# Optimization experiments

Hardware: AMD Instinct MI355X
Metric: run time of the kernel (lower is better)

Reference implementation:

```python
import jax, jax.numpy as jnp
from jax import lax
import numpy as np

B, C, L = 32, 8, 512
C_IN = 512      # must equal L (tokenConv consumes permuted tensor)
D_MODEL = 512
SCALE_NUM = 64  # 63 actual scales


def build_wavelet_bank(scale_num, LB=-8.0, UB=8.0, N=1024, Fb=2.0, Fc=8.0):
    """Replicates cmor_torch; returns centered zero-padded kernel bank [S, K].
    Zero-centering is exact because every kernel length (16*s+1) is odd and K is odd,
    so the padded conv with pad=(K-1)//2 equals the original per-scale conv with
    pad=(k-1)//2."""
    x = np.linspace(LB, UB, N)
    wav = (np.pi * Fb) ** (-0.5) * np.exp(2j * np.pi * Fc * x) * np.exp(-x ** 2 / Fb)
    step = x[1] - x[0]
    kernels = []
    for scale in np.arange(1, scale_num):
        j = (np.arange(scale * (x[-1] - x[0]) + 1) / (scale * step)).astype(int)
        j = j[j < wav.size]
        kernels.append(np.real(wav[j]) * scale ** (-0.5))
    K = max(len(k) for k in kernels)
    if K % 2 == 0:
        K += 1
    bank = np.zeros((len(kernels), K), np.float32)
    for i, k in enumerate(kernels):
        assert (K - len(k)) % 2 == 0, "kernel parity mismatch"
        off = (K - len(k)) // 2
        bank[i, off:off + len(k)] = k
    return bank


def setup_inputs() -> dict:
    key = jax.random.key(0)
    k1, k2 = jax.random.split(key)
    x = jax.random.normal(k1, (B, C, L), dtype=jnp.float32)
    wavelet_bank = jnp.asarray(build_wavelet_bank(SCALE_NUM))  # [63, K]
    token_w = jax.random.normal(k2, (D_MODEL, C_IN, 3), dtype=jnp.float32) * 0.02
    return {"x": x, "wavelet_bank": wavelet_bank, "token_w": token_w}


def reference(x, wavelet_bank, token_w):
    Bb, Cc, Ll = x.shape
    S, K = wavelet_bank.shape
    pad = (K - 1) // 2
    # fused CWT over all (channel, scale) pairs: [B*C, 1, L] conv [S, 1, K] -> [B*C, S, L]
    xr = x.reshape(Bb * Cc, 1, Ll)
    conv = lax.conv_general_dilated(
        xr, wavelet_bank[:, None, :], window_strides=(1,),
        padding=[(pad, pad)], dimension_numbers=("NCH", "OIH", "NCH"))
    d = jnp.abs(jnp.diff(conv, axis=-1))                 # [B*C, S, L-1]
    d = jnp.concatenate([d, d[..., -1:]], axis=-1)       # replicate last sample -> L
    feats = d.reshape(Bb, Cc * S, Ll)
    out = jnp.concatenate([x, feats], axis=1)            # [B, C*(1+S), L]
    # tokenConv on permuted tensor: channels = L (= c_in), length = C*(1+S)
    h = out.transpose(0, 2, 1)                           # [B, L, C_total]
    hp = jnp.concatenate([h[..., -1:], h, h[..., :1]], axis=-1)  # circular pad=1
    y = lax.conv_general_dilated(
        hp, token_w, window_strides=(1,), padding="VALID",
        dimension_numbers=("NCH", "OIH", "NCH"))         # [B, d_model, C_total]
    return y.transpose(0, 2, 1)                          # [B, C_total, d_model]
```

## Files before the change

kernel.cpp:

```cpp
#include <hip/hip_runtime.h>
#include <hip/hip_bf16.h>

#define NB 32
#define NC 8
#define NL 512
#define NS 63
#define NK 1009
#define NPAD 504
#define ND 512
#define NCT 512
#define NROWS 514

typedef __attribute__((ext_vector_type(4))) float f32x4;
typedef __attribute__((ext_vector_type(8))) short short8;

#define APAD_BYTES (NB * NROWS * NL * 2)
#define WB_BYTES   (3 * ND * NL * 2)

typedef const __attribute__((address_space(1))) unsigned int* gp1_t;
typedef __attribute__((address_space(3))) unsigned int* lp3_t;
__device__ __forceinline__ void gload_lds16(const void* g, void* l) {
  __builtin_amdgcn_global_load_lds((gp1_t)g, (lp3_t)l, 16, 0, 0);
}

__device__ __forceinline__ unsigned short bf16_bits(float v) {
  return __builtin_bit_cast(unsigned short, __float2bfloat16(v));
}

#define WAITVM(N) asm volatile("s_waitcnt vmcnt(" #N ")" ::: "memory")
#define FENCE() asm volatile("" ::: "memory")
#define BAR() __builtin_amdgcn_s_barrier()

__global__ __launch_bounds__(256) void prep_kernel(
    const float* __restrict__ bank, const float* __restrict__ tw,
    __hip_bfloat16* __restrict__ Wb, __hip_bfloat16* __restrict__ bankB) {
  const int idx = blockIdx.x * 256 + threadIdx.x;

  {
    int i0 = idx * 4;
    const float4* t4 = (const float4*)(tw + (size_t)i0 * 3);
    float4 a = t4[0], bq = t4[1], c4 = t4[2];
    ushort4 w0 = make_ushort4(bf16_bits(a.x), bf16_bits(a.w), bf16_bits(bq.z), bf16_bits(c4.y));
    ushort4 w1 = make_ushort4(bf16_bits(a.y), bf16_bits(bq.x), bf16_bits(bq.w), bf16_bits(c4.z));
    ushort4 w2 = make_ushort4(bf16_bits(a.z), bf16_bits(bq.y), bf16_bits(c4.x), bf16_bits(c4.w));
    *(ushort4*)(Wb + 0 * ND * NL + i0) = w0;
    *(ushort4*)(Wb + 1 * ND * NL + i0) = w1;
    *(ushort4*)(Wb + 2 * ND * NL + i0) = w2;
  }
  {
    int s = idx >> 10, k = idx & 1023;
    float v = (s < NS && k < NK) ? bank[s * NK + k] : 0.f;
    bankB[idx] = __float2bfloat16(v);
  }
}

#define CPY8_STRIDE 3152

__global__ __launch_bounds__(512) void cwt_kernel(
    const float* __restrict__ x, const __hip_bfloat16* __restrict__ bankB,
    __hip_bfloat16* __restrict__ Apad) {
  __shared__ __align__(16) char smem[8 * 16384 + 8 * CPY8_STRIDE];
  char* bankS = smem;
  char* cpy = smem + 8 * 16384;

  const int tid = threadIdx.x;
  const int bc = blockIdx.x;
  const int b = bc >> 3, c = bc & 7;
  const int w = tid >> 6, l = tid & 63;
  const int hi = l >> 4, li = l & 15;
  const int r8 = l & 7;

  const float* xrow = x + bc * NL;

  if (tid < 512) {
    __hip_bfloat16 v = __float2bfloat16(xrow[tid]);
    Apad[((size_t)(b * NROWS) + 1 + c) * NL + tid] = v;
    if (c == 0) Apad[((size_t)(b * NROWS) + 513) * NL + tid] = v;
  }

  for (int i = 0; i < 13; ++i) {
    int p = tid + i * 512;
    if (p < 6176) {
      int r_ = p / 772;
      int pe = p - r_ * 772;
      int g0 = 2 * pe;
      int i0 = g0 - 8 + r_;
      float xa = (i0 >= NPAD && i0 < NPAD + NL) ? xrow[i0 - NPAD] : 0.f;
      float xb = (i0 + 1 >= NPAD && i0 + 1 < NPAD + NL) ? xrow[i0 + 1 - NPAD] : 0.f;
      float xc = (i0 + 2 >= NPAD && i0 + 2 < NPAD + NL) ? xrow[i0 + 2 - NPAD] : 0.f;
      unsigned u = (unsigned)bf16_bits(xb - xa) | ((unsigned)bf16_bits(xc - xb) << 16);
      *(unsigned*)(cpy + r_ * CPY8_STRIDE + g0 * 2) = u;
    }
  }

#define STAGE(kt)                                                             \
  {                                                                           \
    for (int i = 0; i < 2; ++i) {                                             \
      int ck = tid + i * 512;                                                 \
      int s_ = ck >> 4, rb = ck & 15;                                         \
      int srcc = rb ^ (s_ & 7);                                               \
      gload_lds16(bankB + s_ * 1024 + (kt) * 128 + srcc * 8,                  \
                  bankS + (kt) * 16384 + ck * 16);                            \
    }                                                                         \
  }

#define AVMM(kt, ksl, m)                                                       \
  {                                                                            \
    int srow = (m) * 16 + li;                                                  \
    int chunk = ((ksl) * 4 + hi) ^ (srow & 7);                                 \
    short8 av = *(const short8*)(bankS + (kt) * 16384 + srow * 256 + chunk * 16); \
    _Pragma("unroll") for (int n = 0; n < 4; ++n)                              \
      acc[m][n] = __builtin_amdgcn_mfma_f32_16x16x32_bf16(av, bv[n],           \
                                                          acc[m][n], 0, 0, 0); \
  }

#define CCOMP(kt, M0, M1, M2, M3)                                              \
  {                                                                            \
    _Pragma("unroll") for (int ksl = 0; ksl < 4; ++ksl) {                      \
      short8 bv[4];                                                            \
      _Pragma("unroll") for (int n = 0; n < 4; ++n) {                          \
        int ebyte = 16 + 2 * (tbase + n * 16 + 8 * (li >> 3) +                 \
                              (kt) * 128 + ksl * 32 + 8 * hi);                 \
        bv[n] = *(const short8*)(cpy + r8 * CPY8_STRIDE + ebyte);              \
      }                                                                        \
      if (M0) AVMM(kt, ksl, 0);                                                \
      if (M1) AVMM(kt, ksl, 1);                                                \
      if (M2) AVMM(kt, ksl, 2);                                                \
      if (M3) AVMM(kt, ksl, 3);                                                \
    }                                                                          \
  }

  STAGE(0); STAGE(1); STAGE(2); STAGE(3);
  STAGE(4); STAGE(5); STAGE(6); STAGE(7);

  f32x4 acc[4][4] = {};
  const int tbase = w * 64;

  asm volatile("s_waitcnt vmcnt(14) lgkmcnt(0)" ::: "memory");
  BAR(); FENCE(); CCOMP(0, 0, 0, 1, 1);
  WAITVM(12); BAR(); FENCE(); CCOMP(1, 0, 1, 1, 1);
  WAITVM(10); BAR(); FENCE(); CCOMP(2, 1, 1, 1, 1);
  WAITVM(8);  BAR(); FENCE(); CCOMP(3, 1, 1, 1, 1);
  WAITVM(6);  BAR(); FENCE(); CCOMP(4, 1, 1, 1, 1);
  WAITVM(4);  BAR(); FENCE(); CCOMP(5, 0, 1, 1, 1);
  WAITVM(2);  BAR(); FENCE(); CCOMP(6, 0, 0, 1, 1);
  WAITVM(0);  BAR(); FENCE(); CCOMP(7, 0, 0, 0, 1);

#pragma unroll
  for (int m = 0; m < 4; ++m) {
#pragma unroll
    for (int rg = 0; rg < 4; ++rg) {
      int s = m * 16 + hi * 4 + rg;
      if (s >= NS) continue;
      int ch = 8 + c * NS + s;
      size_t rowbase = ((size_t)(b * NROWS) + 1 + ch) * NL;
#pragma unroll
      for (int n = 0; n < 4; ++n) {
        int t = tbase + n * 16 + li;
        float d = fabsf(acc[m][n][rg]);
        __hip_bfloat16 hv = __float2bfloat16(d);
        bool lastgrp = (w == 7 && n == 3);
        bool skip = lastgrp && (li == 15);
        bool dup = lastgrp && (li == 14);
        if (!skip) Apad[rowbase + t] = hv;
        if (dup) Apad[rowbase + 511] = hv;
        if (ch == NCT - 1) {
          size_t wrapbase = (size_t)(b * NROWS) * NL;
          if (!skip) Apad[wrapbase + t] = hv;
          if (dup) Apad[wrapbase + 511] = hv;
        }
      }
    }
  }
#undef STAGE
#undef AVMM
#undef CCOMP
}

__global__ __launch_bounds__(256) void gemm_kernel(
    const __hip_bfloat16* __restrict__ Ap, const __hip_bfloat16* __restrict__ Wb,
    float* __restrict__ out) {
  __shared__ __hip_bfloat16 sA[4][128 * 32];
  __shared__ __hip_bfloat16 sB[4][128 * 32];

  const int tid = threadIdx.x;
  const int gid = blockIdx.x;
  const int q = gid >> 3;
  const int pid = (gid & 7) * 16 + (q >> 2);
  const int b = pid >> 2;
  const int p0 = (pid & 3) * 128;
  const int o0 = (q & 3) * 128;

  const int w = tid >> 6, lane = tid & 63;
  const int wm = w >> 1, wn = w & 1;
  const int row_in = lane & 15, hi = lane >> 4;

  const int r0 = tid >> 2, cg0 = (tid & 3) ^ ((r0 >> 1) & 3);
  const int ck1 = tid + 256;
  const int r1 = ck1 >> 2, cg1 = (ck1 & 3) ^ ((r1 >> 1) & 3);

#define GSTAGE(kk, bu)                                                         \
  {                                                                            \
    const int kap_ = (kk) >> 4;                                                \
    const int l0_ = ((kk) & 15) << 5;                                          \
    gload_lds16(Ap + ((b * NROWS + p0 + kap_ + r0) * NL + l0_ + cg0 * 8),      \
                &sA[bu][tid * 8]);                                             \
    gload_lds16(Ap + ((b * NROWS + p0 + kap_ + r1) * NL + l0_ + cg1 * 8),      \
                &sA[bu][ck1 * 8]);                                             \
    gload_lds16(Wb + ((kap_ * ND + o0 + r0) * NL + l0_ + cg0 * 8),             \
                &sB[bu][tid * 8]);                                             \
    gload_lds16(Wb + ((kap_ * ND + o0 + r1) * NL + l0_ + cg1 * 8),             \
                &sB[bu][ck1 * 8]);                                             \
  }

#define COMPUTE(bu)                                                            \
  {                                                                            \
    short8 av[4], bv[4];                                                       \
    _Pragma("unroll") for (int m = 0; m < 4; ++m) {                            \
      int row = wm * 64 + m * 16 + row_in;                                     \
      int slot = row * 4 + (hi ^ ((row >> 1) & 3));                            \
      av[m] = *(const short8*)(&sA[bu][slot * 8]);                             \
    }                                                                          \
    _Pragma("unroll") for (int n = 0; n < 4; ++n) {                            \
      int row = wn * 64 + n * 16 + row_in;                                     \
      int slot = row * 4 + (hi ^ ((row >> 1) & 3));                            \
      bv[n] = *(const short8*)(&sB[bu][slot * 8]);                             \
    }                                                                          \
    _Pragma("unroll") for (int m = 0; m < 4; ++m)                              \
      _Pragma("unroll") for (int n = 0; n < 4; ++n)                            \
        acc[m][n] = __builtin_amdgcn_mfma_f32_16x16x32_bf16(av[m], bv[n],      \
                                                            acc[m][n], 0, 0, 0); \
  }

  f32x4 acc[4][4] = {};

  GSTAGE(0, 0);
  GSTAGE(1, 1);

  for (int g = 0; g < 11; ++g) {
    const int kk = g * 4;
    GSTAGE(kk + 2, 2); WAITVM(8); BAR(); FENCE(); COMPUTE(0);
    GSTAGE(kk + 3, 3); WAITVM(8); BAR(); FENCE(); COMPUTE(1);
    GSTAGE(kk + 4, 0); WAITVM(8); BAR(); FENCE(); COMPUTE(2);
    GSTAGE(kk + 5, 1); WAITVM(8); BAR(); FENCE(); COMPUTE(3);
  }
  GSTAGE(46, 2); WAITVM(8); BAR(); FENCE(); COMPUTE(0);
  GSTAGE(47, 3); WAITVM(8); BAR(); FENCE(); COMPUTE(1);
  WAITVM(4); BAR(); FENCE(); COMPUTE(2);
  WAITVM(0); BAR(); FENCE(); COMPUTE(3);
#undef GSTAGE
#undef COMPUTE

#pragma unroll
  for (int m = 0; m < 4; ++m) {
    const int p = p0 + wm * 64 + m * 16 + hi * 4;
#pragma unroll
    for (int n = 0; n < 4; ++n) {
      const int o = o0 + wn * 64 + n * 16 + row_in;
#pragma unroll
      for (int r = 0; r < 4; ++r)
        out[(size_t)((b * NCT) + p + r) * ND + o] = acc[m][n][r];
    }
  }
}

extern "C" void kernel_launch(void* const* d_in, const int* in_sizes, int n_in,
                              void* d_out, int out_size, void* d_ws, size_t ws_size,
                              hipStream_t stream) {
  const float* x = (const float*)d_in[0];
  const float* bank = (const float*)d_in[1];
  const float* tw = (const float*)d_in[2];
  float* out = (float*)d_out;

  char* ws = (char*)d_ws;
  __hip_bfloat16* Apad = (__hip_bfloat16*)ws;
  __hip_bfloat16* Wb = (__hip_bfloat16*)(ws + APAD_BYTES);
  __hip_bfloat16* bankB = (__hip_bfloat16*)(ws + APAD_BYTES + WB_BYTES);

  prep_kernel<<<256, 256, 0, stream>>>(bank, tw, Wb, bankB);
  cwt_kernel<<<256, 512, 0, stream>>>(x, bankB, Apad);
  gemm_kernel<<<512, 256, 0, stream>>>(Apad, Wb, out);
}
```

Before: 60.52 us.

## Enlarge GEMM tile to 256x128 with K=64, triple buffering and MFMA priority

The GEMM kernel now uses 512-thread blocks computing 256x128 output tiles with K-steps of 64, three LDS buffers instead of four, and a rewritten XOR swizzle for 8 chunks per row. It also raises wave priority around MFMA bursts with s_setprio. The goal is more reuse of each B tile and fewer barriers per unit of work. In exchange, LDS use grows to about 144KB per block and only 256 blocks launch, which lowers occupancy and may leave the CUs less evenly loaded.

```diff
diff --git a/kernel.cpp b/kernel.cpp
--- a/kernel.cpp
+++ b/kernel.cpp
@@ -30,6 +30,8 @@
 #define WAITVM(N) asm volatile("s_waitcnt vmcnt(" #N ")" ::: "memory")
 #define FENCE() asm volatile("" ::: "memory")
 #define BAR() __builtin_amdgcn_s_barrier()
+#define PRIO1() __builtin_amdgcn_s_setprio(1)
+#define PRIO0() __builtin_amdgcn_s_setprio(0)
 
 __global__ __launch_bounds__(256) void prep_kernel(
     const float* __restrict__ bank, const float* __restrict__ tw,
@@ -177,79 +179,85 @@
 #undef CCOMP
 }
 
-__global__ __launch_bounds__(256) void gemm_kernel(
+__global__ __launch_bounds__(512) void gemm_kernel(
     const __hip_bfloat16* __restrict__ Ap, const __hip_bfloat16* __restrict__ Wb,
     float* __restrict__ out) {
-  __shared__ __hip_bfloat16 sA[4][128 * 32];
-  __shared__ __hip_bfloat16 sB[4][128 * 32];
+  __shared__ __hip_bfloat16 sA[3][256 * 64];
+  __shared__ __hip_bfloat16 sB[3][128 * 64];
 
   const int tid = threadIdx.x;
   const int gid = blockIdx.x;
-  const int q = gid >> 3;
-  const int pid = (gid & 7) * 16 + (q >> 2);
-  const int b = pid >> 2;
-  const int p0 = (pid & 3) * 128;
-  const int o0 = (q & 3) * 128;
+  const int idx = gid >> 3;
+  const int mblk = (gid & 7) * 8 + (idx & 7);
+  const int nblk = idx >> 3;
+  const int b = mblk >> 1;
+  const int p0 = (mblk & 1) * 256;
+  const int o0 = nblk * 128;
 
   const int w = tid >> 6, lane = tid & 63;
   const int wm = w >> 1, wn = w & 1;
   const int row_in = lane & 15, hi = lane >> 4;
 
-  const int r0 = tid >> 2, cg0 = (tid & 3) ^ ((r0 >> 1) & 3);
-  const int ck1 = tid + 256;
-  const int r1 = ck1 >> 2, cg1 = (ck1 & 3) ^ ((r1 >> 1) & 3);
-
-#define GSTAGE(kk, bu)                                                         \
-  {                                                                            \
-    const int kap_ = (kk) >> 4;                                                \
-    const int l0_ = ((kk) & 15) << 5;                                          \
-    gload_lds16(Ap + ((b * NROWS + p0 + kap_ + r0) * NL + l0_ + cg0 * 8),      \
-                &sA[bu][tid * 8]);                                             \
-    gload_lds16(Ap + ((b * NROWS + p0 + kap_ + r1) * NL + l0_ + cg1 * 8),      \
-                &sA[bu][ck1 * 8]);                                             \
-    gload_lds16(Wb + ((kap_ * ND + o0 + r0) * NL + l0_ + cg0 * 8),             \
-                &sB[bu][tid * 8]);                                             \
-    gload_lds16(Wb + ((kap_ * ND + o0 + r1) * NL + l0_ + cg1 * 8),             \
-                &sB[bu][ck1 * 8]);                                             \
-  }
-
-#define COMPUTE(bu)                                                            \
+#define GSTAGE(kt, bu)                                                         \
+  {                                                                            \
+    const int kap_ = (kt) >> 3;                                                \
+    const int l0_ = ((kt) & 7) << 6;                                           \
+    _Pragma("unroll") for (int i = 0; i < 4; ++i) {                            \
+      int ck = tid + i * 512;                                                  \
+      int row = ck >> 3, cg = (ck & 7) ^ (row & 7);                            \
+      gload_lds16(Ap + ((b * NROWS + p0 + kap_ + row) * NL + l0_ + cg * 8),    \
+                  &sA[bu][ck * 8]);                                            \
+    }                                                                          \
+    _Pragma("unroll") for (int i = 0; i < 2; ++i) {                            \
+      int ck = tid + i * 512;                                                  \
+      int row = ck >> 3, cg = (ck & 7) ^ (row & 7);                            \
+      gload_lds16(Wb + ((kap_ * ND + o0 + row) * NL + l0_ + cg * 8),           \
+                  &sB[bu][ck * 8]);                                            \
+    }                                                                          \
+  }
+
+#define KSLICE(bu, ks)                                                         \
   {                                                                            \
     short8 av[4], bv[4];                                                       \
     _Pragma("unroll") for (int m = 0; m < 4; ++m) {                            \
       int row = wm * 64 + m * 16 + row_in;                                     \
-      int slot = row * 4 + (hi ^ ((row >> 1) & 3));                            \
-      av[m] = *(const short8*)(&sA[bu][slot * 8]);                             \
+      int cs = ((ks) * 4 + hi) ^ (row & 7);                                    \
+      av[m] = *(const short8*)(&sA[bu][(row * 8 + cs) * 8]);                   \
     }                                                                          \
     _Pragma("unroll") for (int n = 0; n < 4; ++n) {                            \
       int row = wn * 64 + n * 16 + row_in;                                     \
-      int slot = row * 4 + (hi ^ ((row >> 1) & 3));                            \
-      bv[n] = *(const short8*)(&sB[bu][slot * 8]);                             \
-    }                                                                          \
+      int cs = ((ks) * 4 + hi) ^ (row & 7);                                    \
+      bv[n] = *(const short8*)(&sB[bu][(row * 8 + cs) * 8]);                   \
+    }                                                                          \
+    PRIO1();                                                                   \
     _Pragma("unroll") for (int m = 0; m < 4; ++m)                              \
       _Pragma("unroll") for (int n = 0; n < 4; ++n)                            \
         acc[m][n] = __builtin_amdgcn_mfma_f32_16x16x32_bf16(av[m], bv[n],      \
                                                             acc[m][n], 0, 0, 0); \
-  }
+    PRIO0();                                                                   \
+  }
+
+#define STEP(kt, bu, bs)                                                       \
+  WAITVM(6); BAR(); FENCE();                                                   \
+  GSTAGE((kt) + 2, bs);                                                        \
+  KSLICE(bu, 0); KSLICE(bu, 1); FENCE();
 
   f32x4 acc[4][4] = {};
 
-  GSTAGE(0, 0);
-  GSTAGE(1, 1);
-
-  for (int g = 0; g < 11; ++g) {
-    const int kk = g * 4;
-    GSTAGE(kk + 2, 2); WAITVM(8); BAR(); FENCE(); COMPUTE(0);
-    GSTAGE(kk + 3, 3); WAITVM(8); BAR(); FENCE(); COMPUTE(1);
-    GSTAGE(kk + 4, 0); WAITVM(8); BAR(); FENCE(); COMPUTE(2);
-    GSTAGE(kk + 5, 1); WAITVM(8); BAR(); FENCE(); COMPUTE(3);
-  }
-  GSTAGE(46, 2); WAITVM(8); BAR(); FENCE(); COMPUTE(0);
-  GSTAGE(47, 3); WAITVM(8); BAR(); FENCE(); COMPUTE(1);
-  WAITVM(4); BAR(); FENCE(); COMPUTE(2);
-  WAITVM(0); BAR(); FENCE(); COMPUTE(3);
+  GSTAGE(0, 0); GSTAGE(1, 1);
+
+  for (int g = 0; g < 7; ++g) {
+    const int kt = g * 3;
+    STEP(kt + 0, 0, 2);
+    STEP(kt + 1, 1, 0);
+    STEP(kt + 2, 2, 1);
+  }
+  STEP(21, 0, 2);
+  WAITVM(6); BAR(); FENCE(); KSLICE(1, 0); KSLICE(1, 1); FENCE();
+  WAITVM(0); BAR(); FENCE(); KSLICE(2, 0); KSLICE(2, 1);
 #undef GSTAGE
-#undef COMPUTE
+#undef KSLICE
+#undef STEP
 
 #pragma unroll
   for (int m = 0; m < 4; ++m) {
@@ -279,5 +287,5 @@
 
   prep_kernel<<<256, 256, 0, stream>>>(bank, tw, Wb, bankB);
   cwt_kernel<<<256, 512, 0, stream>>>(x, bankB, Apad);
-  gemm_kernel<<<512, 256, 0, stream>>>(Apad, Wb, out);
-}
+  gemm_kernel<<<256, 512, 0, stream>>>(Apad, Wb, out);
+}
```

Measured after the change: 59.11 us. 1.02x faster.
